# Optimization experiments

Hardware: AMD Instinct MI355X
Metric: run time of the kernel (lower is better)

The kernel has to match this reference:

```python
import jax, jax.numpy as jnp
import numpy as np

K = 20  # number of unrolled RNN steps (init arg k)


def setup_inputs() -> dict:
    key = jax.random.key(0)
    k1, k2, k3, k4, k5 = jax.random.split(key, 5)
    B, d, H = 2048, 256, 256
    w = jax.random.normal(k1, (B, d, d), dtype=jnp.float32) * 0.1
    b = jax.random.normal(k2, (B, d), dtype=jnp.float32)
    # params (random instead of eye/zeros init so the math is fully exercised)
    Ww = jax.random.normal(k3, (H, d), dtype=jnp.float32) * 0.05
    Wu = jax.random.normal(k4, (H, H), dtype=jnp.float32) * 0.05
    Wv = jax.random.normal(k5, (d, H), dtype=jnp.float32) * 0.05
    return {"w": w, "b": b, "Ww": Ww, "Wu": Wu, "Wv": Wv}


def reference(w, b, Ww, Wu, Wv):
    # w: [B, d, d], b: [B, d]; x_init/h_init default to zeros, return_all=False
    B, d = b.shape
    H = Ww.shape[0]
    x0 = jnp.zeros((B, d), dtype=b.dtype)
    h0 = jnp.zeros((B, H), dtype=b.dtype)

    def step(carry, _):
        x, h = carry
        gradient = jnp.einsum('bij,bj->bi', w, x) - b        # [B, d]
        h = h @ Wu.T + (-gradient) @ Ww.T                     # [B, H]
        h = jax.nn.relu(h)
        x = x + h @ Wv.T                                      # [B, d]
        return (x, h), None

    (x, h), _ = jax.lax.scan(step, (x0, h0), None, length=K)
    return x
```

## Files before the change

### kernel.cpp

```cpp
#include <hip/hip_runtime.h>

typedef _Float16 h2v __attribute__((ext_vector_type(2)));
typedef _Float16 h4v __attribute__((ext_vector_type(4)));
typedef _Float16 h8v __attribute__((ext_vector_type(8)));
typedef float    f4v __attribute__((ext_vector_type(4)));
typedef unsigned int u32;
typedef unsigned long long u64;

#define WUP_STRIDE 264

#define WT_FRAG_STRIDE 1040
#define WT0_OFF   0
#define WT1_OFF   16640
#define TT0_OFF   33280
#define TT1_OFF   51712
#define TT_STRIDE 36
#define WWS0_OFF  70144
#define GC_OFF    0
#define GC_STRIDE 264
#define VS_OFF    135168
#define LDS_FUSED 139264

__device__ inline f4v mfma16(h8v a, h8v b, f4v c) {
  return __builtin_amdgcn_mfma_f32_16x16x32_f16(a, b, c, 0, 0, 0);
}

__device__ inline u64 cvt4(f4v v) {
  h4v d; d[0] = (_Float16)v[0]; d[1] = (_Float16)v[1];
  d[2] = (_Float16)v[2]; d[3] = (_Float16)v[3];
  return __builtin_bit_cast(u64, d);
}

#define BAR() { asm volatile("s_waitcnt lgkmcnt(0)" ::: "memory"); \
                __builtin_amdgcn_s_barrier(); \
                asm volatile("" ::: "memory"); }

#define LDH(basep, kk, dst) { \
    h4v lo_ = *(const h4v*)((basep) + (kk)*32 + 4*g); \
    h4v hi_ = *(const h4v*)((basep) + (kk)*32 + 16 + 4*g); \
    dst = __builtin_shufflevector(lo_, hi_, 0, 1, 2, 3, 4, 5, 6, 7); }

__global__ void prep_k(const float* __restrict__ Wu, _Float16* __restrict__ wup)
{
  int j = blockIdx.x, k = threadIdx.x;
  wup[j * WUP_STRIDE + k] = (_Float16)Wu[j * 256 + k];
  if (k < 8) wup[j * WUP_STRIDE + 256 + k] = (_Float16)0.f;
}

__global__ void prep2_k(const float* __restrict__ Wv, const float* __restrict__ Ww,
                        _Float16* __restrict__ wvp, _Float16* __restrict__ wwp2)
{
  int b = blockIdx.x;
  int tid = threadIdx.x;
  int lane = tid & 63, q = tid >> 6;
  int g2 = (lane >> 4) & 3, l15 = lane & 15;
  if (b < 128) {
    int nt = b >> 3, kk = b & 7;
    int j = nt * 16 + l15;
    _Float16* dst = wvp + ((size_t)(b * 64 + lane)) * 8;
#pragma unroll
    for (int e = 0; e < 2; ++e) {
      int h = 2 * q + e;
      int k = kk * 32 + (h < 4 ? 4 * g2 + h : 16 + 4 * g2 + (h - 4));
      dst[h] = (_Float16)Wv[(size_t)k * 256 + j];
    }
  } else {
    int s = b - 128;
    int it = s & 15;
    int tau = s >> 4;
    int i = it * 16 + l15;
    _Float16* dst = wwp2 + ((size_t)(s * 64 + lane)) * 8;
#pragma unroll
    for (int e = 0; e < 2; ++e) {
      int h = 2 * q + e;
      int t = tau * 32 + (h < 4 ? 4 * g2 + h : 16 + 4 * g2 + (h - 4));
      dst[h] = (_Float16)Ww[(size_t)i * 256 + t];
    }
  }
}

__global__ void matvec8_k(const float* __restrict__ M, const float* __restrict__ V,
                          float* __restrict__ out)
{
  __shared__ float vb[8][256];
  const int i = threadIdx.x;
  const int b0 = blockIdx.x * 8;
#pragma unroll
  for (int r = 0; r < 8; ++r)
    vb[r][i] = V[(size_t)(b0 + r) * 256 + i];
  __syncthreads();
  float acc[8];
#pragma unroll
  for (int r = 0; r < 8; ++r) acc[r] = 0.f;
#pragma unroll 4
  for (int j = 0; j < 256; j += 4) {
    f4v m = *(const f4v*)(M + (size_t)i * 256 + j);
#pragma unroll
    for (int r = 0; r < 8; ++r) {
      f4v v = *(const f4v*)(&vb[r][j]);
      acc[r] += m[0] * v[0] + m[1] * v[1] + m[2] * v[2] + m[3] * v[3];
    }
  }
#pragma unroll
  for (int r = 0; r < 8; ++r)
    out[(size_t)(b0 + r) * 256 + i] = acc[r];
}

__global__ __launch_bounds__(1024, 1) void fused_k(
    const float* __restrict__ w, const _Float16* __restrict__ wvp,
    const _Float16* __restrict__ wwp2, const _Float16* __restrict__ wup,
    const float* __restrict__ beta, float* __restrict__ cout)
{
  extern __shared__ char smem[];

  const int tid = threadIdx.x;
  const int wv = tid >> 6, lane = tid & 63;
  const int g = (lane >> 4) & 3, l15 = lane & 15;
  const int st_t = tid >> 5;
  const int st_c = (tid & 31) * 8;
  const int B   = blockIdx.x;
  const float* wb = w + (size_t)B * 65536;

  const int c_   = tid & 31;
  const int wt_woff = ((c_ >> 2) * 2 + (st_t >> 4)) * WT_FRAG_STRIDE
                    + ((c_ & 1) * 32 + (st_t & 15)) * 16 + ((c_ >> 1) & 1) * 8;
#define WT_WRITE(off) { char* fb_ = smem + (off) + wt_woff; \
    *(u64*)fb_ = cvt4(sw[0]); *(u64*)(fb_ + 256) = cvt4(sw[1]); }

  f4v sw[2];
  uint4 sws;

  h8v bfv[8];
#pragma unroll
  for (int kk = 0; kk < 8; ++kk)
    bfv[kk] = *(const h8v*)(wvp + ((size_t)((wv * 8 + kk) * 64 + lane)) * 8);

  {
    const float* src0 = wb + (size_t)st_t * 256 + st_c;
    sw[0] = *(const f4v*)(src0);
    sw[1] = *(const f4v*)(src0 + 4);
    WT_WRITE(WT0_OFF);
    *(uint4*)(smem + WWS0_OFF + tid * 16) =
        *(const uint4*)((const char*)wwp2 + tid * 16);
    const float* src1 = wb + (size_t)(32 + st_t) * 256 + st_c;
    sw[0] = *(const f4v*)(src1);
    sw[1] = *(const f4v*)(src1 + 4);
    sws = *(const uint4*)((const char*)wwp2 + 16384 + tid * 16);
    BAR();
  }

  f4v acc2[16];
#pragma unroll
  for (int it = 0; it < 16; ++it) acc2[it] = f4v{0.f, 0.f, 0.f, 0.f};

#pragma unroll
  for (int tau = 0; tau < 8; ++tau) {
    if (tau < 7) {
      WT_WRITE(((tau + 1) & 1) ? WT1_OFF : WT0_OFF);
      *(uint4*)(smem + WWS0_OFF + ((tau + 1) % 3) * 16384 + tid * 16) = sws;
    }
    if (tau < 6) {
      const float* src = wb + (size_t)((tau + 2) * 32 + st_t) * 256 + st_c;
      sw[0] = *(const f4v*)(src);
      sw[1] = *(const f4v*)(src + 4);
      sws = *(const uint4*)((const char*)wwp2 + (size_t)(tau + 2) * 16384 + tid * 16);
    }
    __builtin_amdgcn_s_setprio(1);
    if (tau > 0) {
      const _Float16* ttr = (const _Float16*)(smem + (((tau - 1) & 1) ? TT1_OFF : TT0_OFF));
      h8v a0p; LDH(ttr + (wv * 16 + l15) * TT_STRIDE, 0, a0p);
      const char* wws = smem + WWS0_OFF + ((tau - 1) % 3) * 16384;
#pragma unroll
      for (int it = 0; it < 16; ++it) {
        h8v bf = *(const h8v*)(wws + (it * 64 + lane) * 16);
        acc2[it] = mfma16(a0p, bf, acc2[it]);
      }
    }
    f4v acc1[2];
    acc1[0] = f4v{0.f, 0.f, 0.f, 0.f};
    acc1[1] = f4v{0.f, 0.f, 0.f, 0.f};
    {
      const char* wtc = smem + ((tau & 1) ? WT1_OFF : WT0_OFF);
#pragma unroll
      for (int kk = 0; kk < 8; ++kk) {
        h8v a0 = *(const h8v*)(wtc + (kk * 2) * WT_FRAG_STRIDE + lane * 16);
        h8v a1 = *(const h8v*)(wtc + (kk * 2 + 1) * WT_FRAG_STRIDE + lane * 16);
        acc1[0] = mfma16(a0, bfv[kk], acc1[0]);
        acc1[1] = mfma16(a1, bfv[kk], acc1[1]);
      }
    }
    __builtin_amdgcn_s_setprio(0);
    {
      _Float16* ttw = (_Float16*)(smem + ((tau & 1) ? TT1_OFF : TT0_OFF));
#pragma unroll
      for (int tm = 0; tm < 2; ++tm) {
        f4v a = acc1[tm];
        h4v t4; t4[0] = (_Float16)a[0]; t4[1] = (_Float16)a[1];
        t4[2] = (_Float16)a[2]; t4[3] = (_Float16)a[3];
        *(h4v*)(ttw + (wv * 16 + l15) * TT_STRIDE + tm * 16 + g * 4) = t4;
      }
    }
    BAR();
  }

  {
    const _Float16* ttr = (const _Float16*)(smem + TT1_OFF);
    h8v a0p; LDH(ttr + (wv * 16 + l15) * TT_STRIDE, 0, a0p);
    const char* wws = smem + WWS0_OFF + (7 % 3) * 16384;
#pragma unroll
    for (int it = 0; it < 16; ++it) {
      h8v bf = *(const h8v*)(wws + (it * 64 + lane) * 16);
      acc2[it] = mfma16(a0p, bf, acc2[it]);
    }
  }
  BAR();

  {
    _Float16* const GC = (_Float16*)(smem + GC_OFF);
#pragma unroll
    for (int it = 0; it < 16; ++it) {
      const int i = it * 16 + l15;
      f4v a = acc2[it];
      h4v t4; t4[0] = (_Float16)a[0]; t4[1] = (_Float16)a[1];
      t4[2] = (_Float16)a[2]; t4[3] = (_Float16)a[3];
      *(h4v*)(GC + (size_t)i * GC_STRIDE + wv * 16 + g * 4) = t4;
    }
  }
  if (tid < 256) ((u64*)(smem + VS_OFF))[tid] = 0ull;
  BAR();

  h8v af[16];
  {
    const int arow = wv * 16 + l15;
    const _Float16* wurow = wup + (size_t)arow * WUP_STRIDE;
#pragma unroll
    for (int kk = 0; kk < 8; ++kk) { LDH(wurow, kk, af[kk]); }
    const _Float16* gcrow = (const _Float16*)(smem + GC_OFF) + (size_t)arow * GC_STRIDE;
#pragma unroll
    for (int kk = 0; kk < 8; ++kk) { LDH(gcrow, kk, af[8 + kk]); }
  }
  f4v beta4 = *(const f4v*)(beta + (size_t)B * 256 + wv * 16 + 4 * g);
  f4v cm4 = f4v{0.f, 0.f, 0.f, 0.f};

  const int vslot = (wv >> 1) * 64 + g * 16 + (wv & 1) * 8;

  for (int t = 0; t < 20; ++t) {
    const char* vsr = smem + VS_OFF + (t & 1) * 2048;
    f4v c0 = f4v{0.f, 0.f, 0.f, 0.f}, c1 = f4v{0.f, 0.f, 0.f, 0.f};
    f4v c2 = f4v{0.f, 0.f, 0.f, 0.f}, c3 = f4v{0.f, 0.f, 0.f, 0.f};
    __builtin_amdgcn_s_setprio(1);
#pragma unroll
    for (int kk = 0; kk < 16; kk += 4) {
      h8v v0 = *(const h8v*)(vsr + kk * 64 + g * 16);
      h8v v1 = *(const h8v*)(vsr + (kk + 1) * 64 + g * 16);
      h8v v2 = *(const h8v*)(vsr + (kk + 2) * 64 + g * 16);
      h8v v3 = *(const h8v*)(vsr + (kk + 3) * 64 + g * 16);
      c0 = mfma16(af[kk], v0, c0);
      c1 = mfma16(af[kk + 1], v1, c1);
      c2 = mfma16(af[kk + 2], v2, c2);
      c3 = mfma16(af[kk + 3], v3, c3);
    }
    __builtin_amdgcn_s_setprio(0);
    f4v y4 = (c0 + c1) + (c2 + c3);
#pragma unroll
    for (int r = 0; r < 4; ++r) {
      float y = beta4[r] + y4[r] * 128.f;
      float hv = fmaxf(y, 0.f);
      cm4[r] += hv;
      y4[r] = hv;
    }
    char* vsw = smem + VS_OFF + ((t + 1) & 1) * 2048;
    if (l15 == 0) {
      h4v hh, ch;
#pragma unroll
      for (int r = 0; r < 4; ++r) {
        hh[r] = (_Float16)(y4[r] * 0.0078125f);
        ch[r] = (_Float16)(-cm4[r] * 0.0078125f);
      }
      *(u64*)(vsw + vslot)       = __builtin_bit_cast(u64, hh);
      *(u64*)(vsw + 512 + vslot) = __builtin_bit_cast(u64, ch);
    }
    BAR();
  }
  if (l15 == 0)
    *(f4v*)(cout + (size_t)B * 256 + wv * 16 + 4 * g) = cm4;
}

extern "C" void kernel_launch(void* const* d_in, const int* in_sizes, int n_in,
                              void* d_out, int out_size, void* d_ws, size_t ws_size,
                              hipStream_t stream)
{
  const float* w  = (const float*)d_in[0];
  const float* b  = (const float*)d_in[1];
  const float* Ww = (const float*)d_in[2];
  const float* Wu = (const float*)d_in[3];
  const float* Wv = (const float*)d_in[4];

  char* ws = (char*)d_ws;
  float*    beta = (float*)(ws);
  float*    cbuf = (float*)(ws + (size_t)2 * 1024 * 1024);
  _Float16* wvp  = (_Float16*)(ws + (size_t)4 * 1024 * 1024);
  _Float16* wwp2 = (_Float16*)(ws + (size_t)4 * 1024 * 1024 + 131072);
  _Float16* wup  = (_Float16*)(ws + (size_t)4 * 1024 * 1024 + 262144);

  (void)in_sizes; (void)n_in; (void)out_size; (void)ws_size;

  hipFuncSetAttribute((const void*)fused_k,
                      hipFuncAttributeMaxDynamicSharedMemorySize, LDS_FUSED);

  prep_k<<<256, 256, 0, stream>>>(Wu, wup);
  prep2_k<<<256, 256, 0, stream>>>(Wv, Ww, wvp, wwp2);
  matvec8_k<<<256, 256, 0, stream>>>(Ww, b, beta);
  fused_k<<<2048, 1024, LDS_FUSED, stream>>>(w, wvp, wwp2, wup, beta, cbuf);
  matvec8_k<<<256, 256, 0, stream>>>(Wv, cbuf, (float*)d_out);
}
```

Baseline: 422.2 us.

## Process two pipeline stages per barrier with a four-slot LDS ring

Deepens the LDS staging of the w tiles and Ww slices from two or three slots to a four-slot ring and preloads two stages up front. Each loop iteration now processes two tau stages between barriers. The intermediate TT tile becomes a single buffer, written and then read by the same wave. This halves the number of workgroup barriers and the associated pipeline drains, at the cost of more LDS and a longer register-live region.

```diff
diff --git a/kernel.cpp b/kernel.cpp
--- a/kernel.cpp
+++ b/kernel.cpp
@@ -10,16 +10,14 @@
 #define WUP_STRIDE 264
 
 #define WT_FRAG_STRIDE 1040
-#define WT0_OFF   0
-#define WT1_OFF   16640
-#define TT0_OFF   33280
-#define TT1_OFF   51712
+#define WT_SLOT(s) ((s) * 16640)
+#define TT_OFF    66560
 #define TT_STRIDE 36
-#define WWS0_OFF  70144
+#define WWS_OFF   84992
 #define GC_OFF    0
 #define GC_STRIDE 264
 #define VS_OFF    135168
-#define LDS_FUSED 139264
+#define LDS_FUSED 150528
 
 __device__ inline f4v mfma16(h8v a, h8v b, f4v c) {
   return __builtin_amdgcn_mfma_f32_16x16x32_f16(a, b, c, 0, 0, 0);
@@ -112,6 +110,7 @@
     const float* __restrict__ beta, float* __restrict__ cout)
 {
   extern __shared__ char smem[];
+  _Float16* const TT = (_Float16*)(smem + TT_OFF);
 
   const int tid = threadIdx.x;
   const int wv = tid >> 6, lane = tid & 63;
@@ -139,13 +138,19 @@
     const float* src0 = wb + (size_t)st_t * 256 + st_c;
     sw[0] = *(const f4v*)(src0);
     sw[1] = *(const f4v*)(src0 + 4);
-    WT_WRITE(WT0_OFF);
-    *(uint4*)(smem + WWS0_OFF + tid * 16) =
+    WT_WRITE(WT_SLOT(0));
+    *(uint4*)(smem + WWS_OFF + tid * 16) =
         *(const uint4*)((const char*)wwp2 + tid * 16);
     const float* src1 = wb + (size_t)(32 + st_t) * 256 + st_c;
     sw[0] = *(const f4v*)(src1);
     sw[1] = *(const f4v*)(src1 + 4);
-    sws = *(const uint4*)((const char*)wwp2 + 16384 + tid * 16);
+    WT_WRITE(WT_SLOT(1));
+    *(uint4*)(smem + WWS_OFF + 16384 + tid * 16) =
+        *(const uint4*)((const char*)wwp2 + 16384 + tid * 16);
+    const float* src2 = wb + (size_t)(64 + st_t) * 256 + st_c;
+    sw[0] = *(const f4v*)(src2);
+    sw[1] = *(const f4v*)(src2 + 4);
+    sws = *(const uint4*)((const char*)wwp2 + 2 * 16384 + tid * 16);
     BAR();
   }
 
@@ -154,33 +159,23 @@
   for (int it = 0; it < 16; ++it) acc2[it] = f4v{0.f, 0.f, 0.f, 0.f};
 
 #pragma unroll
-  for (int tau = 0; tau < 8; ++tau) {
-    if (tau < 7) {
-      WT_WRITE(((tau + 1) & 1) ? WT1_OFF : WT0_OFF);
-      *(uint4*)(smem + WWS0_OFF + ((tau + 1) % 3) * 16384 + tid * 16) = sws;
-    }
-    if (tau < 6) {
-      const float* src = wb + (size_t)((tau + 2) * 32 + st_t) * 256 + st_c;
+  for (int p = 0; p < 4; ++p) {
+    const int tA = 2 * p, tB = 2 * p + 1;
+    if (p < 3) {
+      WT_WRITE(WT_SLOT((tA + 2) & 3));
+      *(uint4*)(smem + WWS_OFF + ((tA + 2) & 3) * 16384 + tid * 16) = sws;
+    }
+    if (p < 3) {
+      const float* src = wb + (size_t)((tB + 2) * 32 + st_t) * 256 + st_c;
       sw[0] = *(const f4v*)(src);
       sw[1] = *(const f4v*)(src + 4);
-      sws = *(const uint4*)((const char*)wwp2 + (size_t)(tau + 2) * 16384 + tid * 16);
-    }
-    __builtin_amdgcn_s_setprio(1);
-    if (tau > 0) {
-      const _Float16* ttr = (const _Float16*)(smem + (((tau - 1) & 1) ? TT1_OFF : TT0_OFF));
-      h8v a0p; LDH(ttr + (wv * 16 + l15) * TT_STRIDE, 0, a0p);
-      const char* wws = smem + WWS0_OFF + ((tau - 1) % 3) * 16384;
-#pragma unroll
-      for (int it = 0; it < 16; ++it) {
-        h8v bf = *(const h8v*)(wws + (it * 64 + lane) * 16);
-        acc2[it] = mfma16(a0p, bf, acc2[it]);
-      }
+      sws = *(const uint4*)((const char*)wwp2 + (size_t)(tB + 2) * 16384 + tid * 16);
     }
     f4v acc1[2];
     acc1[0] = f4v{0.f, 0.f, 0.f, 0.f};
     acc1[1] = f4v{0.f, 0.f, 0.f, 0.f};
     {
-      const char* wtc = smem + ((tau & 1) ? WT1_OFF : WT0_OFF);
+      const char* wtc = smem + WT_SLOT(tA & 3);
 #pragma unroll
       for (int kk = 0; kk < 8; ++kk) {
         h8v a0 = *(const h8v*)(wtc + (kk * 2) * WT_FRAG_STRIDE + lane * 16);
@@ -189,31 +184,64 @@
         acc1[1] = mfma16(a1, bfv[kk], acc1[1]);
       }
     }
+#pragma unroll
+    for (int tm = 0; tm < 2; ++tm) {
+      f4v a = acc1[tm];
+      h4v t4; t4[0] = (_Float16)a[0]; t4[1] = (_Float16)a[1];
+      t4[2] = (_Float16)a[2]; t4[3] = (_Float16)a[3];
+      *(h4v*)(TT + (wv * 16 + l15) * TT_STRIDE + tm * 16 + g * 4) = t4;
+    }
+    if (p < 3) {
+      WT_WRITE(WT_SLOT((tB + 2) & 3));
+      *(uint4*)(smem + WWS_OFF + ((tB + 2) & 3) * 16384 + tid * 16) = sws;
+    }
+    if (p < 2) {
+      const float* src = wb + (size_t)((tA + 4) * 32 + st_t) * 256 + st_c;
+      sw[0] = *(const f4v*)(src);
+      sw[1] = *(const f4v*)(src + 4);
+      sws = *(const uint4*)((const char*)wwp2 + (size_t)(tA + 4) * 16384 + tid * 16);
+    }
+    __builtin_amdgcn_s_setprio(1);
+    {
+      h8v a0p; LDH(TT + (wv * 16 + l15) * TT_STRIDE, 0, a0p);
+      const char* wws = smem + WWS_OFF + (tA & 3) * 16384;
+#pragma unroll
+      for (int it = 0; it < 16; ++it) {
+        h8v bf = *(const h8v*)(wws + (it * 64 + lane) * 16);
+        acc2[it] = mfma16(a0p, bf, acc2[it]);
+      }
+    }
+    acc1[0] = f4v{0.f, 0.f, 0.f, 0.f};
+    acc1[1] = f4v{0.f, 0.f, 0.f, 0.f};
+    {
+      const char* wtc = smem + WT_SLOT(tB & 3);
+#pragma unroll
+      for (int kk = 0; kk < 8; ++kk) {
+        h8v a0 = *(const h8v*)(wtc + (kk * 2) * WT_FRAG_STRIDE + lane * 16);
+        h8v a1 = *(const h8v*)(wtc + (kk * 2 + 1) * WT_FRAG_STRIDE + lane * 16);
+        acc1[0] = mfma16(a0, bfv[kk], acc1[0]);
+        acc1[1] = mfma16(a1, bfv[kk], acc1[1]);
+      }
+    }
     __builtin_amdgcn_s_setprio(0);
+#pragma unroll
+    for (int tm = 0; tm < 2; ++tm) {
+      f4v a = acc1[tm];
+      h4v t4; t4[0] = (_Float16)a[0]; t4[1] = (_Float16)a[1];
+      t4[2] = (_Float16)a[2]; t4[3] = (_Float16)a[3];
+      *(h4v*)(TT + (wv * 16 + l15) * TT_STRIDE + tm * 16 + g * 4) = t4;
+    }
     {
-      _Float16* ttw = (_Float16*)(smem + ((tau & 1) ? TT1_OFF : TT0_OFF));
-#pragma unroll
-      for (int tm = 0; tm < 2; ++tm) {
-        f4v a = acc1[tm];
-        h4v t4; t4[0] = (_Float16)a[0]; t4[1] = (_Float16)a[1];
-        t4[2] = (_Float16)a[2]; t4[3] = (_Float16)a[3];
-        *(h4v*)(ttw + (wv * 16 + l15) * TT_STRIDE + tm * 16 + g * 4) = t4;
+      h8v a0p; LDH(TT + (wv * 16 + l15) * TT_STRIDE, 0, a0p);
+      const char* wws = smem + WWS_OFF + (tB & 3) * 16384;
+#pragma unroll
+      for (int it = 0; it < 16; ++it) {
+        h8v bf = *(const h8v*)(wws + (it * 64 + lane) * 16);
+        acc2[it] = mfma16(a0p, bf, acc2[it]);
       }
     }
     BAR();
   }
-
-  {
-    const _Float16* ttr = (const _Float16*)(smem + TT1_OFF);
-    h8v a0p; LDH(ttr + (wv * 16 + l15) * TT_STRIDE, 0, a0p);
-    const char* wws = smem + WWS0_OFF + (7 % 3) * 16384;
-#pragma unroll
-    for (int it = 0; it < 16; ++it) {
-      h8v bf = *(const h8v*)(wws + (it * 64 + lane) * 16);
-      acc2[it] = mfma16(a0p, bf, acc2[it]);
-    }
-  }
-  BAR();
 
   {
     _Float16* const GC = (_Float16*)(smem + GC_OFF);
```

Result: slower. 513.5 us (+21.6%).
